# Kernel optimization log

Measured on AMD Instinct MI355X. Metric: run time of the kernel, lower is better.

## Reference

```python
import jax, jax.numpy as jnp
import numpy as np
from jax import lax

B, T, I, H = 256, 1024, 64, 128  # batch(padded_length), seq_len, input_size, hidden_size


def setup_inputs() -> dict:
    key = jax.random.key(0)
    k0, k1, k2, k3, k4 = jax.random.split(key, 5)
    s = 1.0 / np.sqrt(H)  # pytorch LSTM default init scale
    return {
        "data": jax.random.normal(k0, (B, T, I), dtype=jnp.float32),
        "W_ih": jax.random.uniform(k1, (4 * H, I), dtype=jnp.float32, minval=-s, maxval=s),
        "W_hh": jax.random.uniform(k2, (4 * H, H), dtype=jnp.float32, minval=-s, maxval=s),
        "b_ih": jax.random.uniform(k3, (4 * H,), dtype=jnp.float32, minval=-s, maxval=s),
        "b_hh": jax.random.uniform(k4, (4 * H,), dtype=jnp.float32, minval=-s, maxval=s),
    }


def reference(data, W_ih, W_hh, b_ih, b_hh):
    # data: [B, T, I]. Original permutes to [T, B, I] and runs a per-timestep
    # single-layer LSTM loop with zero initial state, collecting h_t each step.
    b, t, _ = data.shape
    h_dim = W_hh.shape[1]
    # Precompute input projection for all timesteps: [T, B, 4H]
    xs = jnp.einsum('bti,gi->tbg', data, W_ih) + b_ih + b_hh

    def step(carry, x_t):
        h, c = carry
        gates = x_t + h @ W_hh.T  # [B, 4H]
        i, f, g, o = jnp.split(gates, 4, axis=-1)  # pytorch gate order: i,f,g,o
        i = jax.nn.sigmoid(i)
        f = jax.nn.sigmoid(f)
        g = jnp.tanh(g)
        o = jax.nn.sigmoid(o)
        c = f * c + i * g
        h = o * jnp.tanh(c)
        return (h, c), h

    h0 = jnp.zeros((b, h_dim), dtype=data.dtype)
    _, hs = lax.scan(step, (h0, h0), xs)  # hs: [T, B, H]
    return jnp.transpose(hs, (1, 0, 2))  # [B, T, H]
```

## Files before the change

kernel.cpp:

```cpp
#include <hip/hip_runtime.h>


typedef _Float16 half8  __attribute__((ext_vector_type(8)));
typedef _Float16 half2t __attribute__((ext_vector_type(2)));
typedef float  floatx4  __attribute__((ext_vector_type(4)));
typedef int    intx4   __attribute__((ext_vector_type(4)));

constexpr int Tt = 1024;
constexpr int Ii = 64;
constexpr int Hh = 128;
constexpr int CH = 16;
constexpr int NCH = Tt / CH;

__device__ __forceinline__ float fast_rcp(float x) { return __builtin_amdgcn_rcpf(x); }
__device__ __forceinline__ float exp2_(float x)    { return __builtin_amdgcn_exp2f(x); }
__device__ __forceinline__ half2t pk16(float a, float b) {
    return __builtin_bit_cast(half2t, __builtin_amdgcn_cvt_pkrtz(a, b));
}
#define MFMA16(A, B, C) __builtin_amdgcn_mfma_f32_16x16x32_f16((A), (B), (C), 0, 0, 0)
#define MFMAI8(A, B, C) __builtin_amdgcn_mfma_i32_16x16x64_i8((A), (B), (C), 0, 0, 0)
union H8U { half8 v; half2t p[4]; };

__device__ __forceinline__ half8 cvt8(float4 a, float4 b) {
    H8U u;
    u.p[0] = pk16(a.x, a.y); u.p[1] = pk16(a.z, a.w);
    u.p[2] = pk16(b.x, b.y); u.p[3] = pk16(b.z, b.w);
    return u.v;
}
__device__ __forceinline__ floatx4 splat4(float a) { floatx4 r = {a, a, a, a}; return r; }

__device__ __forceinline__ int pkq4(const float* s, float qs) {
    const int a = (int)rintf(s[0] * qs) & 255;
    const int b = (int)rintf(s[1] * qs) & 255;
    const int c = (int)rintf(s[2] * qs) & 255;
    const int d = (int)rintf(s[3] * qs) & 255;
    return a | (b << 8) | (c << 16) | (d << 24);
}

__global__ __launch_bounds__(512, 1) void lstm_i8r2(
    const float* __restrict__ data,
    const float* __restrict__ W_ih,
    const float* __restrict__ W_hh,
    const float* __restrict__ b_ih,
    const float* __restrict__ b_hh,
    float* __restrict__ out)
{
    const int b   = blockIdx.x;
    const int t   = threadIdx.x;
    const int w   = t >> 6;
    const int l   = t & 63;
    const int col = l & 15;
    const int kg  = l >> 4;

    __shared__ __align__(16) half8 wihf[8][512];
    __shared__ __align__(16) signed char hbq[2][Hh];
    if (t < Hh) hbq[0][t] = 0;

    intx4 bqh[4][2];
    float dqh[4];
    float bs[4];
#pragma unroll
    for (int g = 0; g < 4; ++g) {
        const float sc = (g == 2) ? -2.8853900817779268f : -1.4426950408889634f;
        const int row = 128 * g + 16 * w + col;
        bs[g] = sc * (b_ih[row] + b_hh[row]);
        const float* wh = W_hh + (size_t)row * Hh;
        const float* wi = W_ih + (size_t)row * Ii;
        float mw = 1e-20f;
#pragma unroll
        for (int k = 0; k < Hh; k += 4) {
            const float4 f = *(const float4*)(wh + k);
            mw = fmaxf(mw, fmaxf(fmaxf(fabsf(f.x), fabsf(f.y)),
                                 fmaxf(fabsf(f.z), fabsf(f.w))));
        }
        const float qs = 127.f / mw;
        dqh[g] = sc * mw * (1.f / (127.f * 127.f));
#pragma unroll
        for (int s = 0; s < 2; ++s) {
            const float* src = wh + 64 * s + 16 * kg;
            intx4 q;
            q[0] = pkq4(src + 0,  qs);
            q[1] = pkq4(src + 4,  qs);
            q[2] = pkq4(src + 8,  qs);
            q[3] = pkq4(src + 12, qs);
            bqh[g][s] = q;
        }
#pragma unroll
        for (int s = 0; s < 2; ++s) {
            const float* src = wi + 32 * s + 8 * kg;
            const float4 f0 = ((const float4*)src)[0];
            const float4 f1 = ((const float4*)src)[1];
            H8U u;
            u.p[0] = pk16(sc * f0.x, sc * f0.y); u.p[1] = pk16(sc * f0.z, sc * f0.w);
            u.p[2] = pk16(sc * f1.x, sc * f1.y); u.p[3] = pk16(sc * f1.z, sc * f1.w);
            wihf[g * 2 + s][t] = u.v;
        }
    }

    const float* xp  = data + (size_t)b * Tt * Ii;
    float*       opr = out  + (size_t)b * Tt * Hh + 16 * w + col;

    const float* xbase = xp + (size_t)(l & 15) * Ii + 8 * kg;
    float4 xf0 = *(const float4*)(xbase);
    float4 xf1 = *(const float4*)(xbase + 4);
    float4 xf2 = *(const float4*)(xbase + 32);
    float4 xf3 = *(const float4*)(xbase + 36);

    float c = 0.0f;
    __syncthreads();

#pragma unroll 1
    for (int n = 0; n < NCH; ++n) {
        floatx4 xw0, xw1, xw2, xw3;
        {
            const half8 ax0 = cvt8(xf0, xf1);
            const half8 ax1 = cvt8(xf2, xf3);
            const int nn = (n + 1 < NCH) ? (n + 1) : n;
            const float* xb2 = xbase + (size_t)nn * CH * Ii;
            xf0 = *(const float4*)(xb2);
            xf1 = *(const float4*)(xb2 + 4);
            xf2 = *(const float4*)(xb2 + 32);
            xf3 = *(const float4*)(xb2 + 36);
            const half8 fA0 = wihf[0][t], fA1 = wihf[1][t];
            const half8 fB0 = wihf[2][t], fB1 = wihf[3][t];
            const half8 fC0 = wihf[4][t], fC1 = wihf[5][t];
            const half8 fD0 = wihf[6][t], fD1 = wihf[7][t];
            xw0 = MFMA16(ax0, fA0, splat4(bs[0]));
            xw1 = MFMA16(ax0, fB0, splat4(bs[1]));
            xw2 = MFMA16(ax0, fC0, splat4(bs[2]));
            xw3 = MFMA16(ax0, fD0, splat4(bs[3]));
            xw0 = MFMA16(ax1, fA1, xw0);
            xw1 = MFMA16(ax1, fB1, xw1);
            xw2 = MFMA16(ax1, fC1, xw2);
            xw3 = MFMA16(ax1, fD1, xw3);
        }

#define STEP(P, R, CUR, XTRA)                                                 \
        {                                                                     \
            const signed char* hbase = &hbq[CUR][16 * kg];                    \
            const intx4 ah0 = *(const intx4*)(hbase);                         \
            const intx4 ah1 = *(const intx4*)(hbase + 64);                    \
            XTRA;                                                             \
            __builtin_amdgcn_s_setprio(1);                                    \
            const intx4 z4 = {0, 0, 0, 0};                                    \
            intx4 qfA = MFMAI8(ah0, bqh[1][0], z4);                 \
            intx4 qgA = MFMAI8(ah0, bqh[2][0], z4);                 \
            intx4 qiA = MFMAI8(ah0, bqh[0][0], z4);                 \
            intx4 qfB = MFMAI8(ah1, bqh[1][1], z4);                 \
            intx4 qgB = MFMAI8(ah1, bqh[2][1], z4);                 \
            intx4 qiB = MFMAI8(ah1, bqh[0][1], z4);                 \
            intx4 qoA = MFMAI8(ah0, bqh[3][0], z4);                 \
            intx4 qoB = MFMAI8(ah1, bqh[3][1], z4);                 \
            const float e_f = exp2_(fmaf((float)(qfA[R] + qfB[R]), dqh[1], xw1[R])); \
            const float e_g = exp2_(fmaf((float)(qgA[R] + qgB[R]), dqh[2], xw2[R])); \
            const float e_i = exp2_(fmaf((float)(qiA[R] + qiB[R]), dqh[0], xw0[R])); \
            __builtin_amdgcn_s_setprio(0);                                    \
            const float fg  = fast_rcp(1.0f + e_f);                           \
            const float igv = (1.0f - e_g) *                                  \
                              fast_rcp((1.0f + e_i) * (1.0f + e_g));          \
            c = fmaf(fg, c, igv);                                             \
            const float e_o = exp2_(fmaf((float)(qoA[R] + qoB[R]), dqh[3], xw3[R])); \
            const float e_c = exp2_(-2.8853900817779268f * c);                \
            const float h   = (1.0f - e_c) *                                  \
                              fast_rcp((1.0f + e_o) * (1.0f + e_c));          \
            if (kg == (P)) {                                                  \
                hbq[(CUR) ^ 1][16 * w + col] =                                \
                    (signed char)(int)rintf(h * 127.f);                       \
                *opr = h;                                                     \
            }                                                                 \
            opr += Hh;                                                        \
            asm volatile("s_waitcnt lgkmcnt(0)\n\ts_barrier" ::: "memory");   \
        }

#define PHASE(P)                                                              \
        STEP(P, 0, 0, c = __shfl(c, (l + 48) & 63))                           \
        STEP(P, 1, 1, (void)0) STEP(P, 2, 0, (void)0) STEP(P, 3, 1, (void)0)

        PHASE(0) PHASE(1) PHASE(2) PHASE(3)
#undef PHASE
#undef STEP
    }
}

extern "C" void kernel_launch(void* const* d_in, const int* in_sizes, int n_in,
                              void* d_out, int out_size, void* d_ws, size_t ws_size,
                              hipStream_t stream) {
    const float* data = (const float*)d_in[0];
    const float* W_ih = (const float*)d_in[1];
    const float* W_hh = (const float*)d_in[2];
    const float* b_ih = (const float*)d_in[3];
    const float* b_hh = (const float*)d_in[4];
    float* out = (float*)d_out;

    hipLaunchKernelGGL(lstm_i8r2, dim3(256), dim3(512), 0, stream,
                       data, W_ih, W_hh, b_ih, b_hh, out);
}
```

Measured before the change: 379.6 us.

## Software-pipeline next chunk's input projection into current chunk's recurrence steps

```diff
diff --git a/kernel.cpp b/kernel.cpp
--- a/kernel.cpp
+++ b/kernel.cpp
@@ -37,7 +37,7 @@
     return a | (b << 8) | (c << 16) | (d << 24);
 }
 
-__global__ __launch_bounds__(512, 1) void lstm_i8r2(
+__global__ __launch_bounds__(512, 1) void lstm_i8r3(
     const float* __restrict__ data,
     const float* __restrict__ W_ih,
     const float* __restrict__ W_hh,
@@ -106,34 +106,37 @@
     float4 xf2 = *(const float4*)(xbase + 32);
     float4 xf3 = *(const float4*)(xbase + 36);
 
+    floatx4 xw0, xw1, xw2, xw3;
+    {
+        const half8 ax0 = cvt8(xf0, xf1);
+        const half8 ax1 = cvt8(xf2, xf3);
+        xf0 = *(const float4*)(xbase + CH * Ii);
+        xf1 = *(const float4*)(xbase + CH * Ii + 4);
+        xf2 = *(const float4*)(xbase + CH * Ii + 32);
+        xf3 = *(const float4*)(xbase + CH * Ii + 36);
+        const half8 fA0 = wihf[0][t], fA1 = wihf[1][t];
+        const half8 fB0 = wihf[2][t], fB1 = wihf[3][t];
+        const half8 fC0 = wihf[4][t], fC1 = wihf[5][t];
+        const half8 fD0 = wihf[6][t], fD1 = wihf[7][t];
+        xw0 = MFMA16(ax0, fA0, splat4(bs[0]));
+        xw1 = MFMA16(ax0, fB0, splat4(bs[1]));
+        xw2 = MFMA16(ax0, fC0, splat4(bs[2]));
+        xw3 = MFMA16(ax0, fD0, splat4(bs[3]));
+        xw0 = MFMA16(ax1, fA1, xw0);
+        xw1 = MFMA16(ax1, fB1, xw1);
+        xw2 = MFMA16(ax1, fC1, xw2);
+        xw3 = MFMA16(ax1, fD1, xw3);
+    }
+
+    half8 nax0, nax1, wA, wB;
+    floatx4 nxw0, nxw1, nxw2, nxw3;
+
     float c = 0.0f;
     __syncthreads();
 
 #pragma unroll 1
     for (int n = 0; n < NCH; ++n) {
-        floatx4 xw0, xw1, xw2, xw3;
-        {
-            const half8 ax0 = cvt8(xf0, xf1);
-            const half8 ax1 = cvt8(xf2, xf3);
-            const int nn = (n + 1 < NCH) ? (n + 1) : n;
-            const float* xb2 = xbase + (size_t)nn * CH * Ii;
-            xf0 = *(const float4*)(xb2);
-            xf1 = *(const float4*)(xb2 + 4);
-            xf2 = *(const float4*)(xb2 + 32);
-            xf3 = *(const float4*)(xb2 + 36);
-            const half8 fA0 = wihf[0][t], fA1 = wihf[1][t];
-            const half8 fB0 = wihf[2][t], fB1 = wihf[3][t];
-            const half8 fC0 = wihf[4][t], fC1 = wihf[5][t];
-            const half8 fD0 = wihf[6][t], fD1 = wihf[7][t];
-            xw0 = MFMA16(ax0, fA0, splat4(bs[0]));
-            xw1 = MFMA16(ax0, fB0, splat4(bs[1]));
-            xw2 = MFMA16(ax0, fC0, splat4(bs[2]));
-            xw3 = MFMA16(ax0, fD0, splat4(bs[3]));
-            xw0 = MFMA16(ax1, fA1, xw0);
-            xw1 = MFMA16(ax1, fB1, xw1);
-            xw2 = MFMA16(ax1, fC1, xw2);
-            xw3 = MFMA16(ax1, fD1, xw3);
-        }
+        const float* xb2 = xbase + (size_t)((n + 2 < NCH) ? n + 2 : NCH - 1) * CH * Ii;
 
 #define STEP(P, R, CUR, XTRA)                                                 \
         {                                                                     \
@@ -154,12 +157,12 @@
             const float e_f = exp2_(fmaf((float)(qfA[R] + qfB[R]), dqh[1], xw1[R])); \
             const float e_g = exp2_(fmaf((float)(qgA[R] + qgB[R]), dqh[2], xw2[R])); \
             const float e_i = exp2_(fmaf((float)(qiA[R] + qiB[R]), dqh[0], xw0[R])); \
+            const float e_o = exp2_(fmaf((float)(qoA[R] + qoB[R]), dqh[3], xw3[R])); \
             __builtin_amdgcn_s_setprio(0);                                    \
             const float fg  = fast_rcp(1.0f + e_f);                           \
             const float igv = (1.0f - e_g) *                                  \
                               fast_rcp((1.0f + e_i) * (1.0f + e_g));          \
             c = fmaf(fg, c, igv);                                             \
-            const float e_o = exp2_(fmaf((float)(qoA[R] + qoB[R]), dqh[3], xw3[R])); \
             const float e_c = exp2_(-2.8853900817779268f * c);                \
             const float h   = (1.0f - e_c) *                                  \
                               fast_rcp((1.0f + e_o) * (1.0f + e_c));          \
@@ -172,13 +175,39 @@
             asm volatile("s_waitcnt lgkmcnt(0)\n\ts_barrier" ::: "memory");   \
         }
 
-#define PHASE(P)                                                              \
-        STEP(P, 0, 0, c = __shfl(c, (l + 48) & 63))                           \
-        STEP(P, 1, 1, (void)0) STEP(P, 2, 0, (void)0) STEP(P, 3, 1, (void)0)
-
-        PHASE(0) PHASE(1) PHASE(2) PHASE(3)
+#define PHASE(P, X0, X1, X2, X3)                                              \
+        STEP(P, 0, 0, X0) STEP(P, 1, 1, X1) STEP(P, 2, 0, X2) STEP(P, 3, 1, X3)
+
+        PHASE(0,
+              (c = __shfl(c, (l + 48) & 63), nax0 = cvt8(xf0, xf1)),
+              nax1 = cvt8(xf2, xf3),
+              (wA = wihf[0][t], wB = wihf[1][t]),
+              (nxw0 = MFMA16(nax0, wA, splat4(bs[0])),
+               nxw0 = MFMA16(nax1, wB, nxw0)))
+        PHASE(1,
+              (c = __shfl(c, (l + 48) & 63), wA = wihf[2][t], wB = wihf[3][t]),
+              (nxw1 = MFMA16(nax0, wA, splat4(bs[1])),
+               nxw1 = MFMA16(nax1, wB, nxw1)),
+              (wA = wihf[4][t], wB = wihf[5][t]),
+              (nxw2 = MFMA16(nax0, wA, splat4(bs[2])),
+               nxw2 = MFMA16(nax1, wB, nxw2)))
+        PHASE(2,
+              (c = __shfl(c, (l + 48) & 63), wA = wihf[6][t], wB = wihf[7][t]),
+              (nxw3 = MFMA16(nax0, wA, splat4(bs[3])),
+               nxw3 = MFMA16(nax1, wB, nxw3)),
+              (xf0 = *(const float4*)(xb2),
+               xf1 = *(const float4*)(xb2 + 4)),
+              (xf2 = *(const float4*)(xb2 + 32),
+               xf3 = *(const float4*)(xb2 + 36)))
+        PHASE(3,
+              c = __shfl(c, (l + 48) & 63),
+              (void)0,
+              (void)0,
+              (void)0)
 #undef PHASE
 #undef STEP
+
+        xw0 = nxw0; xw1 = nxw1; xw2 = nxw2; xw3 = nxw3;
     }
 }
 
@@ -192,6 +221,6 @@
     const float* b_hh = (const float*)d_in[4];
     float* out = (float*)d_out;
 
-    hipLaunchKernelGGL(lstm_i8r2, dim3(256), dim3(512), 0, stream,
+    hipLaunchKernelGGL(lstm_i8r3, dim3(256), dim3(512), 0, stream,
                        data, W_ih, W_hh, b_ih, b_hh, out);
 }
```

After: 375.9 us. No clear change (-1.0%).
